# Performance work log

Hardware: AMD Instinct MI355X
Metric: run time of the kernel (lower is better)

## Reference

```python
import jax, jax.numpy as jnp
import numpy as np

N, E, D_IN, HID, D_OUT, HEADS = 4096, 262144, 256, 256, 128, 4


def gcn_conv(x, edge_index, edge_weight, W, b):
    # PyG GCNConv: linear -> gcn_norm (add self loops, sym norm) -> scatter-add -> +bias
    n = x.shape[0]
    row, col = edge_index[0], edge_index[1]
    loop = jnp.arange(n)
    row_f = jnp.concatenate([row, loop])
    col_f = jnp.concatenate([col, loop])
    ew_f = jnp.concatenate([edge_weight, jnp.ones((n,), edge_weight.dtype)])
    deg = jax.ops.segment_sum(ew_f, col_f, num_segments=n)
    dinv = jnp.where(deg > 0, jax.lax.rsqrt(deg), 0.0)
    norm = dinv[row_f] * ew_f * dinv[col_f]  # [E+N]
    h = x @ W                                # [N, out]
    out = jax.ops.segment_sum(norm[:, None] * h[row_f], col_f, num_segments=n)
    return out + b


def mha(x, in_proj_w, in_proj_b, out_proj_w, out_proj_b):
    # torch.nn.MultiheadAttention, unbatched input [L, Emb], q=k=v=x
    L, Emb = x.shape
    dh = Emb // HEADS
    qkv = x @ in_proj_w.T + in_proj_b
    q, k, v = jnp.split(qkv, 3, axis=-1)
    rs = lambda t: t.reshape(L, HEADS, dh).transpose(1, 0, 2)  # [H, L, dh]
    q, k, v = rs(q), rs(k), rs(v)
    scores = jnp.einsum('hld,hmd->hlm', q, k) / np.float32(np.sqrt(dh))
    attn = jax.nn.softmax(scores, axis=-1)
    o = jnp.einsum('hlm,hmd->hld', attn, v).transpose(1, 0, 2).reshape(L, Emb)
    return o @ out_proj_w.T + out_proj_b


def setup_inputs() -> dict:
    key = jax.random.key(0)
    ks = jax.random.split(key, 12)
    s = 0.02
    return {
        'node_features': jax.random.normal(ks[0], (N, D_IN), jnp.float32),
        'edge_index': jax.random.randint(ks[1], (2, E), 0, N),
        'edge_weight': jax.random.uniform(ks[2], (E,), jnp.float32),
        'W1': jax.random.normal(ks[3], (D_IN, HID), jnp.float32) * s,
        'b1': jnp.zeros((HID,), jnp.float32),
        'W2': jax.random.normal(ks[4], (HID, HID), jnp.float32) * s,
        'b2': jnp.zeros((HID,), jnp.float32),
        'W3': jax.random.normal(ks[5], (HID, D_OUT), jnp.float32) * s,
        'b3': jnp.zeros((D_OUT,), jnp.float32),
        'in_proj_w': jax.random.normal(ks[6], (3 * HID, HID), jnp.float32) * s,
        'in_proj_b': jnp.zeros((3 * HID,), jnp.float32),
        'out_proj_w': jax.random.normal(ks[7], (HID, HID), jnp.float32) * s,
        'out_proj_b': jnp.zeros((HID,), jnp.float32),
    }


def reference(node_features, edge_index, edge_weight, W1, b1, W2, b2, W3, b3,
              in_proj_w, in_proj_b, out_proj_w, out_proj_b):
    ew = edge_weight.astype(jnp.float32)
    x = gcn_conv(node_features, edge_index, ew, W1, b1)
    x = jax.nn.relu(mha(x, in_proj_w, in_proj_b, out_proj_w, out_proj_b))
    # dropout is identity at inference
    x = gcn_conv(x, edge_index, ew, W2, b2)
    x = jax.nn.relu(mha(x, in_proj_w, in_proj_b, out_proj_w, out_proj_b))
    x = gcn_conv(x, edge_index, ew, W3, b3)
    return jax.nn.sigmoid(x)
```

## Files before the change

### kernel.cpp

```cpp
#include <hip/hip_runtime.h>
#include <math.h>

#define N_NODES 4096
#define N_EDGES 262144

typedef __attribute__((ext_vector_type(4))) float f32x4;
typedef __attribute__((ext_vector_type(8))) short s16x8;
typedef __attribute__((ext_vector_type(4))) unsigned short u16x4;

__device__ inline unsigned short f2bf(float f) {
    unsigned u = __builtin_bit_cast(unsigned, f);
    u += 0x7FFF + ((u >> 16) & 1);
    return (unsigned short)(u >> 16);
}
__device__ inline unsigned short f2bf_t(float f) {
    return (unsigned short)(__builtin_bit_cast(unsigned, f) >> 16);
}
__device__ inline float bf2f(unsigned short u) {
    unsigned x = ((unsigned)u) << 16;
    return __builtin_bit_cast(float, x);
}

#define SWZ(row, colb) (((row) << 7) + ((colb) ^ (((row) & 7) << 4)))

__global__ void prep_all(const float* __restrict__ x0, const float* __restrict__ ipw,
                         const float* __restrict__ opw, const float* __restrict__ ipb,
                         const float* __restrict__ W1, const float* __restrict__ W2,
                         const float* __restrict__ W3,
                         unsigned short* __restrict__ x0b, unsigned short* __restrict__ ipwb,
                         unsigned short* __restrict__ opwb, float* __restrict__ ipbs,
                         unsigned short* __restrict__ W1t, unsigned short* __restrict__ W2t,
                         unsigned short* __restrict__ W3t) {
    const int NA = 262144;
    const int NB = 49152;
    const int NC = 16384;
    const int ND1 = 65536, ND2 = 65536, ND3 = 32768;
    const int NE = 768;
    const int total = NA + NB + NC + ND1 + ND2 + ND3 + NE;
    for (int idx = blockIdx.x * blockDim.x + threadIdx.x; idx < total;
         idx += gridDim.x * blockDim.x) {
        int t = idx;
        if (t < NA) {
            int i = t * 4;
            f32x4 v = *(const f32x4*)(x0 + i);
            u16x4 o;
#pragma unroll
            for (int j = 0; j < 4; j++) o[j] = f2bf(v[j]);
            *(u16x4*)(x0b + i) = o;
            continue;
        }
        t -= NA;
        if (t < NB) {
            int i = t * 4;
            int r = i >> 8;
            float sc = (r >= 256 && r < 512) ? 0.1803369f : 1.0f;
            f32x4 v = *(const f32x4*)(ipw + i);
            u16x4 o;
#pragma unroll
            for (int j = 0; j < 4; j++) o[j] = f2bf(v[j] * sc);
            *(u16x4*)(ipwb + i) = o;
            continue;
        }
        t -= NB;
        if (t < NC) {
            int i = t * 4;
            f32x4 v = *(const f32x4*)(opw + i);
            u16x4 o;
#pragma unroll
            for (int j = 0; j < 4; j++) o[j] = f2bf(v[j]);
            *(u16x4*)(opwb + i) = o;
            continue;
        }
        t -= NC;
        if (t < ND1) {
            int r = t & 255, c = t >> 8;
            W1t[c * 256 + r] = f2bf(W1[r * 256 + c]);
            continue;
        }
        t -= ND1;
        if (t < ND2) {
            int r = t & 255, c = t >> 8;
            W2t[c * 256 + r] = f2bf(W2[r * 256 + c]);
            continue;
        }
        t -= ND2;
        if (t < ND3) {
            int r = t & 255, c = t >> 8;
            W3t[c * 256 + r] = f2bf(W3[r * 128 + c]);
            continue;
        }
        t -= ND3;
        {
            float sc = (t >= 256 && t < 512) ? 0.1803369f : 1.0f;
            ipbs[t] = ipb[t] * sc;
        }
    }
}

__global__ void deg_accum(const int* __restrict__ col, const float* __restrict__ ew,
                          float* deg, int* cnt) {
    for (int e = blockIdx.x * blockDim.x + threadIdx.x; e < N_EDGES;
         e += gridDim.x * blockDim.x) {
        int c = col[e];
        atomicAdd(&deg[c], ew[e]);
        atomicAdd(&cnt[c], 1);
    }
}

__global__ __launch_bounds__(1024) void scan_offsets(const int* __restrict__ cnt,
                                                     float* __restrict__ deg,
                                                     int* off, int* fill) {
    __shared__ int s[1024];
    int tid = threadIdx.x;
#pragma unroll
    for (int q = 0; q < 4; q++) {
        int i = tid * 4 + q;
        deg[i] = rsqrtf(deg[i] + 1.0f);
    }
    int c0 = cnt[tid * 4 + 0], c1 = cnt[tid * 4 + 1];
    int c2 = cnt[tid * 4 + 2], c3 = cnt[tid * 4 + 3];
    int lsum = c0 + c1 + c2 + c3;
    s[tid] = lsum;
    __syncthreads();
    for (int d = 1; d < 1024; d <<= 1) {
        int v = (tid >= d) ? s[tid - d] : 0;
        __syncthreads();
        s[tid] += v;
        __syncthreads();
    }
    int incl = s[tid];
    int base = incl - lsum;
    int o0 = base, o1 = base + c0, o2 = base + c0 + c1, o3 = base + c0 + c1 + c2;
    off[tid * 4 + 0] = o0;  fill[tid * 4 + 0] = o0;
    off[tid * 4 + 1] = o1;  fill[tid * 4 + 1] = o1;
    off[tid * 4 + 2] = o2;  fill[tid * 4 + 2] = o2;
    off[tid * 4 + 3] = o3;  fill[tid * 4 + 3] = o3;
    if (tid == 1023) off[4096] = incl;
}

__global__ void scatter_edges(const int* __restrict__ row, const int* __restrict__ col,
                              const float* __restrict__ ew, const float* __restrict__ dinv,
                              int* fill, unsigned long long* __restrict__ ep) {
    for (int e = blockIdx.x * blockDim.x + threadIdx.x; e < N_EDGES;
         e += gridDim.x * blockDim.x) {
        int r = row[e], c = col[e];
        int p = atomicAdd(&fill[c], 1);
        float w = dinv[r] * ew[e] * dinv[c];
        unsigned long long v =
            ((unsigned long long)__builtin_bit_cast(unsigned, w) << 32) | (unsigned)r;
        ep[p] = v;
    }
}

template <bool BIAS, int ACT, bool QKV>
__global__ __launch_bounds__(64) void gemm_bf16(const unsigned short* __restrict__ A,
                                                const unsigned short* __restrict__ B,
                                                const float* __restrict__ bias,
                                                unsigned short* __restrict__ C,
                                                unsigned short* __restrict__ Vt, int P) {
    int lane = threadIdx.x & 63;
    int lx = lane & 15, g = lane >> 4;
    int brow = blockIdx.y * 32, bcol = blockIdx.x * 64;
    const unsigned short* Ap0 = A + (size_t)(brow + lx) * 256 + g * 8;
    const unsigned short* Ap1 = Ap0 + 16 * 256;
    const unsigned short* Bp = B + (size_t)(bcol + lx) * 256 + g * 8;
    f32x4 acc[2][4];
#pragma unroll
    for (int mi = 0; mi < 2; mi++)
#pragma unroll
        for (int nt = 0; nt < 4; nt++) acc[mi][nt] = f32x4{0.f, 0.f, 0.f, 0.f};
#pragma unroll
    for (int kc = 0; kc < 8; kc++) {
        s16x8 a0 = *(const s16x8*)(Ap0 + kc * 32);
        s16x8 a1 = *(const s16x8*)(Ap1 + kc * 32);
#pragma unroll
        for (int nt = 0; nt < 4; nt++) {
            s16x8 b = *(const s16x8*)(Bp + (size_t)nt * 16 * 256 + kc * 32);
            acc[0][nt] = __builtin_amdgcn_mfma_f32_16x16x32_bf16(a0, b, acc[0][nt], 0, 0, 0);
            acc[1][nt] = __builtin_amdgcn_mfma_f32_16x16x32_bf16(a1, b, acc[1][nt], 0, 0, 0);
        }
    }
    bool isV = QKV && (bcol >= 512);
    if (!isV) {
#pragma unroll
        for (int mi = 0; mi < 2; mi++)
#pragma unroll
            for (int nt = 0; nt < 4; nt++)
#pragma unroll
                for (int r = 0; r < 4; r++) {
                    int row = brow + mi * 16 + g * 4 + r, col = bcol + nt * 16 + lx;
                    float v = acc[mi][nt][r];
                    if (BIAS) v += bias[col];
                    if (ACT == 1) v = fmaxf(v, 0.f);
                    C[(size_t)row * P + col] = f2bf(v);
                }
    } else {
        int head = (bcol - 512) >> 6;
#pragma unroll
        for (int mi = 0; mi < 2; mi++)
#pragma unroll
            for (int nt = 0; nt < 4; nt++) {
                int col = bcol + nt * 16 + lx;
                u16x4 vv;
#pragma unroll
                for (int r = 0; r < 4; r++) {
                    float v = acc[mi][nt][r];
                    if (BIAS) v += bias[col];
                    vv[r] = f2bf(v);
                }
                *(u16x4*)(Vt + (size_t)(head * 64 + nt * 16 + lx) * 4096 +
                          brow + mi * 16 + g * 4) = vv;
            }
    }
}

template <int P, bool SIG>
__global__ __launch_bounds__(64) void gcn_agg(const unsigned short* __restrict__ H,
                                              const int* __restrict__ off,
                                              const unsigned long long* __restrict__ ep,
                                              const float* __restrict__ dinv,
                                              const float* __restrict__ bias,
                                              unsigned short* __restrict__ outb,
                                              float* __restrict__ outf) {
    constexpr int CPT = P / 64;
    __shared__ unsigned long long se[64];
    int i = blockIdx.x, tid = threadIdx.x;
    float di = dinv[i];
    float d2 = di * di;
    float acc[CPT];
    if (CPT == 4) {
        u16x4 h = *(const u16x4*)(H + (size_t)i * P + tid * 4);
#pragma unroll
        for (int j = 0; j < 4; j++) acc[j] = d2 * bf2f(h[j]);
    } else {
        unsigned h = *(const unsigned*)(H + (size_t)i * P + tid * 2);
        acc[0] = d2 * bf2f((unsigned short)(h & 0xFFFF));
        acc[1] = d2 * bf2f((unsigned short)(h >> 16));
    }
    int beg = off[i], end = off[i + 1];
    for (int base = beg; base < end; base += 64) {
        int n = min(64, end - base);
        __syncthreads();
        if (tid < n) se[tid] = ep[base + tid];
        __syncthreads();
#pragma unroll 4
        for (int j = 0; j < n; j++) {
            unsigned long long v = se[j];
            int r = (int)(unsigned)v;
            float w = __builtin_bit_cast(float, (unsigned)(v >> 32));
            size_t rb = (size_t)r * P;
            if (CPT == 4) {
                u16x4 h = *(const u16x4*)(H + rb + tid * 4);
#pragma unroll
                for (int q = 0; q < 4; q++) acc[q] += w * bf2f(h[q]);
            } else {
                unsigned h = *(const unsigned*)(H + rb + tid * 2);
                acc[0] += w * bf2f((unsigned short)(h & 0xFFFF));
                acc[1] += w * bf2f((unsigned short)(h >> 16));
            }
        }
    }
#pragma unroll
    for (int j = 0; j < CPT; j++) {
        int c = tid * CPT + j;
        float v = acc[j] + bias[c];
        if (SIG) {
            v = 1.f / (1.f + exp2f(-v * 1.442695f));
            outf[(size_t)i * P + c] = v;
        } else {
            outb[(size_t)i * P + c] = f2bf(v);
        }
    }
}

__global__ __launch_bounds__(256) void attn_mfma(const unsigned short* __restrict__ qkv,
                                                 const unsigned short* __restrict__ Vt,
                                                 unsigned short* __restrict__ Po,
                                                 float* __restrict__ Pl) {
    __shared__ unsigned short Ks[2][64 * 64];
    __shared__ unsigned short Vs[2][64 * 64];
    __shared__ unsigned short Ps[4][16 * 64];

    int tid = threadIdx.x;
    int wid = tid >> 6, lane = tid & 63, g = lane >> 4, lx = lane & 15;
    int head = blockIdx.y, chunk = blockIdx.z;
    int qw = blockIdx.x * 64 + wid * 16;

    s16x8 qa[2];
#pragma unroll
    for (int kc = 0; kc < 2; kc++)
        qa[kc] = *(const s16x8*)(qkv + (size_t)(qw + lx) * 768 + head * 64 + kc * 32 + g * 8);

    int kr0 = tid >> 3, dc0 = tid & 7;
    int kr1 = kr0 + 32;
    int kt_beg = chunk * 16, kt_end = kt_beg + 16;

    const unsigned short* kp0 =
        qkv + 256 + head * 64 + (size_t)(kt_beg * 64 + kr0) * 768 + dc0 * 8;
    const unsigned short* kp1 = kp0 + (size_t)32 * 768;
    const unsigned short* vp0 =
        Vt + (size_t)head * 64 * 4096 + (size_t)kr0 * 4096 + kt_beg * 64 + dc0 * 8;
    const unsigned short* vp1 = vp0 + (size_t)32 * 4096;

    s16x8 stK[2], stV[2];
    auto issue = [&]() {
        stK[0] = *(const s16x8*)kp0;
        stK[1] = *(const s16x8*)kp1;
        stV[0] = *(const s16x8*)vp0;
        stV[1] = *(const s16x8*)vp1;
        kp0 += 64 * 768; kp1 += 64 * 768;
        vp0 += 64; vp1 += 64;
    };
    auto commit = [&](int b) {
        *(s16x8*)((char*)Ks[b] + SWZ(kr0, dc0 * 16)) = stK[0];
        *(s16x8*)((char*)Ks[b] + SWZ(kr1, dc0 * 16)) = stK[1];
        *(s16x8*)((char*)Vs[b] + SWZ(kr0, dc0 * 16)) = stV[0];
        *(s16x8*)((char*)Vs[b] + SWZ(kr1, dc0 * 16)) = stV[1];
    };

    float lreg[4] = {0.f, 0.f, 0.f, 0.f};
    f32x4 o[4];
#pragma unroll
    for (int dt = 0; dt < 4; dt++) o[dt] = f32x4{0.f, 0.f, 0.f, 0.f};

    char* PsW = (char*)Ps[wid];

    issue();
    commit(0);
    __syncthreads();

    for (int kt = kt_beg; kt < kt_end; kt++) {
        int cur = (kt - kt_beg) & 1;
        if (kt + 1 < kt_end) issue();

        f32x4 s4[4];
        __builtin_amdgcn_s_setprio(1);
#pragma unroll
        for (int nt = 0; nt < 4; nt++) {
            f32x4 acc = f32x4{0.f, 0.f, 0.f, 0.f};
#pragma unroll
            for (int kc = 0; kc < 2; kc++) {
                s16x8 kb = *(const s16x8*)((char*)Ks[cur] + SWZ(nt * 16 + lx, kc * 64 + g * 16));
                acc = __builtin_amdgcn_mfma_f32_16x16x32_bf16(qa[kc], kb, acc, 0, 0, 0);
            }
            s4[nt] = acc;
        }
        __builtin_amdgcn_s_setprio(0);

#pragma unroll
        for (int nt = 0; nt < 4; nt++)
#pragma unroll
            for (int r = 0; r < 4; r++) {
                float p = exp2f(fminf(s4[nt][r], 60.f));
                lreg[r] += p;
                *(unsigned short*)(PsW + SWZ(4 * g + r, (nt * 16 + lx) * 2)) = f2bf_t(p);
            }

        __builtin_amdgcn_s_setprio(1);
#pragma unroll
        for (int kc = 0; kc < 2; kc++) {
            s16x8 pa = *(const s16x8*)(PsW + SWZ(lx, kc * 64 + g * 16));
#pragma unroll
            for (int dt = 0; dt < 4; dt++) {
                s16x8 vb = *(const s16x8*)((char*)Vs[cur] + SWZ(dt * 16 + lx, kc * 64 + g * 16));
                o[dt] = __builtin_amdgcn_mfma_f32_16x16x32_bf16(pa, vb, o[dt], 0, 0, 0);
            }
        }
        __builtin_amdgcn_s_setprio(0);

        if (kt + 1 < kt_end) commit(1 - cur);
        __syncthreads();
    }

#pragma unroll
    for (int r = 0; r < 4; r++) {
        float ls = lreg[r];
        ls += __shfl_xor(ls, 1, 16);
        ls += __shfl_xor(ls, 2, 16);
        ls += __shfl_xor(ls, 4, 16);
        ls += __shfl_xor(ls, 8, 16);
        int qrow = qw + 4 * g + r;
        size_t base = (size_t)(chunk * 4 + head) * 4096 + qrow;
        if (lx == 0) Pl[base] = ls;
#pragma unroll
        for (int dt = 0; dt < 4; dt++)
            Po[base * 64 + dt * 16 + lx] = f2bf(o[dt][r]);
    }
}

__global__ __launch_bounds__(256) void attn_combine(const unsigned short* __restrict__ Po,
                                                    const float* __restrict__ Pl,
                                                    unsigned short* __restrict__ att) {
    int tid = threadIdx.x;
    int q = blockIdx.x * 4 + (tid >> 6);
    int lane = tid & 63;
    int head = lane >> 4, quad = lane & 15;
    float L = 0.f;
    f32x4 ov = {0.f, 0.f, 0.f, 0.f};
#pragma unroll
    for (int c = 0; c < 4; c++) {
        size_t base = (size_t)(c * 4 + head) * 4096 + q;
        L += Pl[base];
        u16x4 p = *(const u16x4*)(Po + base * 64 + quad * 4);
#pragma unroll
        for (int k = 0; k < 4; k++) ov[k] += bf2f(p[k]);
    }
    float inv = 1.0f / L;
    u16x4 r;
#pragma unroll
    for (int k = 0; k < 4; k++) r[k] = f2bf(ov[k] * inv);
    *(u16x4*)(att + (size_t)q * 256 + head * 64 + quad * 4) = r;
}

extern "C" void kernel_launch(void* const* d_in, const int* in_sizes, int n_in,
                              void* d_out, int out_size, void* d_ws, size_t ws_size,
                              hipStream_t stream) {
    const float* x0  = (const float*)d_in[0];
    const int*   eix = (const int*)d_in[1];
    const float* ew  = (const float*)d_in[2];
    const float* W1  = (const float*)d_in[3];
    const float* b1  = (const float*)d_in[4];
    const float* W2  = (const float*)d_in[5];
    const float* b2  = (const float*)d_in[6];
    const float* W3  = (const float*)d_in[7];
    const float* b3  = (const float*)d_in[8];
    const float* ipw = (const float*)d_in[9];
    const float* ipb = (const float*)d_in[10];
    const float* opw = (const float*)d_in[11];
    const float* opb = (const float*)d_in[12];
    float* out = (float*)d_out;

    char* ws = (char*)d_ws;
    size_t o = 0;
    auto alloc = [&](size_t bytes) -> void* {
        void* p = ws + o;
        o = (o + bytes + 255) & ~size_t(255);
        return p;
    };
    float* dinv  = (float*)alloc(N_NODES * 4);
    int*   cnt   = (int*)alloc(N_NODES * 4);
    int*   off   = (int*)alloc((N_NODES + 1) * 4);
    int*   fill  = (int*)alloc(N_NODES * 4);
    unsigned long long* ep = (unsigned long long*)alloc((size_t)N_EDGES * 8);
    unsigned short* x0b  = (unsigned short*)alloc((size_t)N_NODES * 256 * 2);
    unsigned short* W1t  = (unsigned short*)alloc(256 * 256 * 2);
    unsigned short* W2t  = (unsigned short*)alloc(256 * 256 * 2);
    unsigned short* W3t  = (unsigned short*)alloc(128 * 256 * 2);
    unsigned short* ipwb = (unsigned short*)alloc(768 * 256 * 2);
    unsigned short* opwb = (unsigned short*)alloc(256 * 256 * 2);
    float* ipbs          = (float*)alloc(768 * 4);
    unsigned short* Hb   = (unsigned short*)alloc((size_t)N_NODES * 256 * 2);
    unsigned short* XAb  = (unsigned short*)alloc((size_t)N_NODES * 256 * 2);
    unsigned short* XBb  = (unsigned short*)alloc((size_t)N_NODES * 256 * 2);
    unsigned short* QKVb = (unsigned short*)alloc((size_t)N_NODES * 768 * 2);
    unsigned short* Vt   = (unsigned short*)alloc((size_t)4 * 64 * 4096 * 2);
    unsigned short* Po   = (unsigned short*)alloc((size_t)16 * 4096 * 64 * 2);
    float* Pl            = (float*)alloc((size_t)16 * 4096 * 4);

    const int* row = eix;
    const int* col = eix + N_EDGES;

    hipMemsetAsync(dinv, 0, N_NODES * 4, stream);
    hipMemsetAsync(cnt, 0, N_NODES * 4, stream);
    prep_all<<<512, 256, 0, stream>>>(x0, ipw, opw, ipb, W1, W2, W3,
                                      x0b, ipwb, opwb, ipbs, W1t, W2t, W3t);
    deg_accum<<<512, 256, 0, stream>>>(col, ew, dinv, cnt);
    scan_offsets<<<1, 1024, 0, stream>>>(cnt, dinv, off, fill);
    scatter_edges<<<512, 256, 0, stream>>>(row, col, ew, dinv, fill, ep);

    gemm_bf16<false, 0, false><<<dim3(4, 128), 64, 0, stream>>>(x0b, W1t, nullptr, Hb, nullptr, 256);
    gcn_agg<256, false><<<N_NODES, 64, 0, stream>>>(Hb, off, ep, dinv, b1, XAb, nullptr);
    gemm_bf16<true, 0, true><<<dim3(12, 128), 64, 0, stream>>>(XAb, ipwb, ipbs, QKVb, Vt, 768);
    attn_mfma<<<dim3(64, 4, 4), 256, 0, stream>>>(QKVb, Vt, Po, Pl);
    attn_combine<<<N_NODES / 4, 256, 0, stream>>>(Po, Pl, Hb);
    gemm_bf16<true, 1, false><<<dim3(4, 128), 64, 0, stream>>>(Hb, opwb, opb, XBb, nullptr, 256);
    gemm_bf16<false, 0, false><<<dim3(4, 128), 64, 0, stream>>>(XBb, W2t, nullptr, Hb, nullptr, 256);
    gcn_agg<256, false><<<N_NODES, 64, 0, stream>>>(Hb, off, ep, dinv, b2, XAb, nullptr);
    gemm_bf16<true, 0, true><<<dim3(12, 128), 64, 0, stream>>>(XAb, ipwb, ipbs, QKVb, Vt, 768);
    attn_mfma<<<dim3(64, 4, 4), 256, 0, stream>>>(QKVb, Vt, Po, Pl);
    attn_combine<<<N_NODES / 4, 256, 0, stream>>>(Po, Pl, Hb);
    gemm_bf16<true, 1, false><<<dim3(4, 128), 64, 0, stream>>>(Hb, opwb, opb, XBb, nullptr, 256);
    gemm_bf16<false, 0, false><<<dim3(2, 128), 64, 0, stream>>>(XBb, W3t, nullptr, Hb, nullptr, 128);
    gcn_agg<128, true><<<N_NODES, 64, 0, stream>>>(Hb, off, ep, dinv, b3, nullptr, out);
}
```

Before: 303.8 us.

## Fold degree accumulation into prep, enlarge GEMM tiles, split GCN edges across warps

Merges the degree/count atomic accumulation into the prep kernel to drop one launch. Enlarges the bf16 GEMM tile from 32 to 64 rows per single-wave block, halving the grid and reusing B fragments over four A fragments. Rewrites GCN aggregation to use four waves per node, each handling a strided subset of edges, followed by a shared-memory reduction. This trades fewer GEMM blocks and more register pressure for more memory-level parallelism in the gather.

```diff
diff --git a/kernel.cpp b/kernel.cpp
--- a/kernel.cpp
+++ b/kernel.cpp
@@ -27,16 +27,19 @@
                          const float* __restrict__ opw, const float* __restrict__ ipb,
                          const float* __restrict__ W1, const float* __restrict__ W2,
                          const float* __restrict__ W3,
+                         const int* __restrict__ col, const float* __restrict__ ew,
                          unsigned short* __restrict__ x0b, unsigned short* __restrict__ ipwb,
                          unsigned short* __restrict__ opwb, float* __restrict__ ipbs,
                          unsigned short* __restrict__ W1t, unsigned short* __restrict__ W2t,
-                         unsigned short* __restrict__ W3t) {
+                         unsigned short* __restrict__ W3t,
+                         float* __restrict__ deg, int* __restrict__ cnt) {
     const int NA = 262144;
     const int NB = 49152;
     const int NC = 16384;
     const int ND1 = 65536, ND2 = 65536, ND3 = 32768;
     const int NE = 768;
-    const int total = NA + NB + NC + ND1 + ND2 + ND3 + NE;
+    const int NG = N_EDGES;
+    const int total = NA + NB + NC + ND1 + ND2 + ND3 + NE + NG;
     for (int idx = blockIdx.x * blockDim.x + threadIdx.x; idx < total;
          idx += gridDim.x * blockDim.x) {
         int t = idx;
@@ -90,20 +93,17 @@
             continue;
         }
         t -= ND3;
-        {
+        if (t < NE) {
             float sc = (t >= 256 && t < 512) ? 0.1803369f : 1.0f;
             ipbs[t] = ipb[t] * sc;
-        }
-    }
-}
-
-__global__ void deg_accum(const int* __restrict__ col, const float* __restrict__ ew,
-                          float* deg, int* cnt) {
-    for (int e = blockIdx.x * blockDim.x + threadIdx.x; e < N_EDGES;
-         e += gridDim.x * blockDim.x) {
-        int c = col[e];
-        atomicAdd(&deg[c], ew[e]);
-        atomicAdd(&cnt[c], 1);
+            continue;
+        }
+        t -= NE;
+        {
+            int c = col[t];
+            atomicAdd(&deg[c], ew[t]);
+            atomicAdd(&cnt[c], 1);
+        }
     }
 }
 
@@ -160,30 +160,34 @@
                                                 unsigned short* __restrict__ Vt, int P) {
     int lane = threadIdx.x & 63;
     int lx = lane & 15, g = lane >> 4;
-    int brow = blockIdx.y * 32, bcol = blockIdx.x * 64;
-    const unsigned short* Ap0 = A + (size_t)(brow + lx) * 256 + g * 8;
-    const unsigned short* Ap1 = Ap0 + 16 * 256;
+    int brow = blockIdx.y * 64, bcol = blockIdx.x * 64;
+    const unsigned short* Ap = A + (size_t)(brow + lx) * 256 + g * 8;
     const unsigned short* Bp = B + (size_t)(bcol + lx) * 256 + g * 8;
-    f32x4 acc[2][4];
-#pragma unroll
-    for (int mi = 0; mi < 2; mi++)
+    f32x4 acc[4][4];
+#pragma unroll
+    for (int mi = 0; mi < 4; mi++)
 #pragma unroll
         for (int nt = 0; nt < 4; nt++) acc[mi][nt] = f32x4{0.f, 0.f, 0.f, 0.f};
 #pragma unroll
     for (int kc = 0; kc < 8; kc++) {
-        s16x8 a0 = *(const s16x8*)(Ap0 + kc * 32);
-        s16x8 a1 = *(const s16x8*)(Ap1 + kc * 32);
-#pragma unroll
-        for (int nt = 0; nt < 4; nt++) {
-            s16x8 b = *(const s16x8*)(Bp + (size_t)nt * 16 * 256 + kc * 32);
-            acc[0][nt] = __builtin_amdgcn_mfma_f32_16x16x32_bf16(a0, b, acc[0][nt], 0, 0, 0);
-            acc[1][nt] = __builtin_amdgcn_mfma_f32_16x16x32_bf16(a1, b, acc[1][nt], 0, 0, 0);
-        }
+        s16x8 a[4], b[4];
+#pragma unroll
+        for (int mi = 0; mi < 4; mi++)
+            a[mi] = *(const s16x8*)(Ap + (size_t)mi * 16 * 256 + kc * 32);
+#pragma unroll
+        for (int nt = 0; nt < 4; nt++)
+            b[nt] = *(const s16x8*)(Bp + (size_t)nt * 16 * 256 + kc * 32);
+#pragma unroll
+        for (int mi = 0; mi < 4; mi++)
+#pragma unroll
+            for (int nt = 0; nt < 4; nt++)
+                acc[mi][nt] = __builtin_amdgcn_mfma_f32_16x16x32_bf16(a[mi], b[nt],
+                                                                      acc[mi][nt], 0, 0, 0);
     }
     bool isV = QKV && (bcol >= 512);
     if (!isV) {
 #pragma unroll
-        for (int mi = 0; mi < 2; mi++)
+        for (int mi = 0; mi < 4; mi++)
 #pragma unroll
             for (int nt = 0; nt < 4; nt++)
 #pragma unroll
@@ -197,7 +201,7 @@
     } else {
         int head = (bcol - 512) >> 6;
 #pragma unroll
-        for (int mi = 0; mi < 2; mi++)
+        for (int mi = 0; mi < 4; mi++)
 #pragma unroll
             for (int nt = 0; nt < 4; nt++) {
                 int col = bcol + nt * 16 + lx;
@@ -215,60 +219,72 @@
 }
 
 template <int P, bool SIG>
-__global__ __launch_bounds__(64) void gcn_agg(const unsigned short* __restrict__ H,
-                                              const int* __restrict__ off,
-                                              const unsigned long long* __restrict__ ep,
-                                              const float* __restrict__ dinv,
-                                              const float* __restrict__ bias,
-                                              unsigned short* __restrict__ outb,
-                                              float* __restrict__ outf) {
+__global__ __launch_bounds__(256) void gcn_agg(const unsigned short* __restrict__ H,
+                                               const int* __restrict__ off,
+                                               const unsigned long long* __restrict__ ep,
+                                               const float* __restrict__ dinv,
+                                               const float* __restrict__ bias,
+                                               unsigned short* __restrict__ outb,
+                                               float* __restrict__ outf) {
     constexpr int CPT = P / 64;
-    __shared__ unsigned long long se[64];
+    __shared__ unsigned long long se[128];
+    __shared__ float red[3][P];
     int i = blockIdx.x, tid = threadIdx.x;
-    float di = dinv[i];
-    float d2 = di * di;
+    int wid = tid >> 6, lane = tid & 63;
     float acc[CPT];
-    if (CPT == 4) {
-        u16x4 h = *(const u16x4*)(H + (size_t)i * P + tid * 4);
-#pragma unroll
-        for (int j = 0; j < 4; j++) acc[j] = d2 * bf2f(h[j]);
-    } else {
-        unsigned h = *(const unsigned*)(H + (size_t)i * P + tid * 2);
-        acc[0] = d2 * bf2f((unsigned short)(h & 0xFFFF));
-        acc[1] = d2 * bf2f((unsigned short)(h >> 16));
+#pragma unroll
+    for (int j = 0; j < CPT; j++) acc[j] = 0.f;
+    if (wid == 0) {
+        float di = dinv[i];
+        float d2 = di * di;
+        if (CPT == 4) {
+            u16x4 h = *(const u16x4*)(H + (size_t)i * P + lane * 4);
+#pragma unroll
+            for (int j = 0; j < 4; j++) acc[j] = d2 * bf2f(h[j]);
+        } else {
+            unsigned h = *(const unsigned*)(H + (size_t)i * P + lane * 2);
+            acc[0] = d2 * bf2f((unsigned short)(h & 0xFFFF));
+            acc[1] = d2 * bf2f((unsigned short)(h >> 16));
+        }
     }
     int beg = off[i], end = off[i + 1];
-    for (int base = beg; base < end; base += 64) {
-        int n = min(64, end - base);
+    for (int base = beg; base < end; base += 128) {
+        int n = min(128, end - base);
         __syncthreads();
         if (tid < n) se[tid] = ep[base + tid];
         __syncthreads();
-#pragma unroll 4
-        for (int j = 0; j < n; j++) {
+        for (int j = wid; j < n; j += 4) {
             unsigned long long v = se[j];
             int r = (int)(unsigned)v;
             float w = __builtin_bit_cast(float, (unsigned)(v >> 32));
             size_t rb = (size_t)r * P;
             if (CPT == 4) {
-                u16x4 h = *(const u16x4*)(H + rb + tid * 4);
+                u16x4 h = *(const u16x4*)(H + rb + lane * 4);
 #pragma unroll
                 for (int q = 0; q < 4; q++) acc[q] += w * bf2f(h[q]);
             } else {
-                unsigned h = *(const unsigned*)(H + rb + tid * 2);
+                unsigned h = *(const unsigned*)(H + rb + lane * 2);
                 acc[0] += w * bf2f((unsigned short)(h & 0xFFFF));
                 acc[1] += w * bf2f((unsigned short)(h >> 16));
             }
         }
     }
-#pragma unroll
-    for (int j = 0; j < CPT; j++) {
-        int c = tid * CPT + j;
-        float v = acc[j] + bias[c];
-        if (SIG) {
-            v = 1.f / (1.f + exp2f(-v * 1.442695f));
-            outf[(size_t)i * P + c] = v;
-        } else {
-            outb[(size_t)i * P + c] = f2bf(v);
+    if (wid > 0) {
+#pragma unroll
+        for (int j = 0; j < CPT; j++) red[wid - 1][lane * CPT + j] = acc[j];
+    }
+    __syncthreads();
+    if (wid == 0) {
+#pragma unroll
+        for (int j = 0; j < CPT; j++) {
+            int c = lane * CPT + j;
+            float v = acc[j] + red[0][c] + red[1][c] + red[2][c] + bias[c];
+            if (SIG) {
+                v = 1.f / (1.f + exp2f(-v * 1.442695f));
+                outf[(size_t)i * P + c] = v;
+            } else {
+                outb[(size_t)i * P + c] = f2bf(v);
+            }
         }
     }
 }
@@ -462,24 +478,23 @@
 
     hipMemsetAsync(dinv, 0, N_NODES * 4, stream);
     hipMemsetAsync(cnt, 0, N_NODES * 4, stream);
-    prep_all<<<512, 256, 0, stream>>>(x0, ipw, opw, ipb, W1, W2, W3,
-                                      x0b, ipwb, opwb, ipbs, W1t, W2t, W3t);
-    deg_accum<<<512, 256, 0, stream>>>(col, ew, dinv, cnt);
+    prep_all<<<512, 256, 0, stream>>>(x0, ipw, opw, ipb, W1, W2, W3, col, ew,
+                                      x0b, ipwb, opwb, ipbs, W1t, W2t, W3t, dinv, cnt);
     scan_offsets<<<1, 1024, 0, stream>>>(cnt, dinv, off, fill);
     scatter_edges<<<512, 256, 0, stream>>>(row, col, ew, dinv, fill, ep);
 
-    gemm_bf16<false, 0, false><<<dim3(4, 128), 64, 0, stream>>>(x0b, W1t, nullptr, Hb, nullptr, 256);
-    gcn_agg<256, false><<<N_NODES, 64, 0, stream>>>(Hb, off, ep, dinv, b1, XAb, nullptr);
-    gemm_bf16<true, 0, true><<<dim3(12, 128), 64, 0, stream>>>(XAb, ipwb, ipbs, QKVb, Vt, 768);
+    gemm_bf16<false, 0, false><<<dim3(4, 64), 64, 0, stream>>>(x0b, W1t, nullptr, Hb, nullptr, 256);
+    gcn_agg<256, false><<<N_NODES, 256, 0, stream>>>(Hb, off, ep, dinv, b1, XAb, nullptr);
+    gemm_bf16<true, 0, true><<<dim3(12, 64), 64, 0, stream>>>(XAb, ipwb, ipbs, QKVb, Vt, 768);
     attn_mfma<<<dim3(64, 4, 4), 256, 0, stream>>>(QKVb, Vt, Po, Pl);
     attn_combine<<<N_NODES / 4, 256, 0, stream>>>(Po, Pl, Hb);
-    gemm_bf16<true, 1, false><<<dim3(4, 128), 64, 0, stream>>>(Hb, opwb, opb, XBb, nullptr, 256);
-    gemm_bf16<false, 0, false><<<dim3(4, 128), 64, 0, stream>>>(XBb, W2t, nullptr, Hb, nullptr, 256);
-    gcn_agg<256, false><<<N_NODES, 64, 0, stream>>>(Hb, off, ep, dinv, b2, XAb, nullptr);
-    gemm_bf16<true, 0, true><<<dim3(12, 128), 64, 0, stream>>>(XAb, ipwb, ipbs, QKVb, Vt, 768);
+    gemm_bf16<true, 1, false><<<dim3(4, 64), 64, 0, stream>>>(Hb, opwb, opb, XBb, nullptr, 256);
+    gemm_bf16<false, 0, false><<<dim3(4, 64), 64, 0, stream>>>(XBb, W2t, nullptr, Hb, nullptr, 256);
+    gcn_agg<256, false><<<N_NODES, 256, 0, stream>>>(Hb, off, ep, dinv, b2, XAb, nullptr);
+    gemm_bf16<true, 0, true><<<dim3(12, 64), 64, 0, stream>>>(XAb, ipwb, ipbs, QKVb, Vt, 768);
     attn_mfma<<<dim3(64, 4, 4), 256, 0, stream>>>(QKVb, Vt, Po, Pl);
     attn_combine<<<N_NODES / 4, 256, 0, stream>>>(Po, Pl, Hb);
-    gemm_bf16<true, 1, false><<<dim3(4, 128), 64, 0, stream>>>(Hb, opwb, opb, XBb, nullptr, 256);
-    gemm_bf16<false, 0, false><<<dim3(2, 128), 64, 0, stream>>>(XBb, W3t, nullptr, Hb, nullptr, 128);
-    gcn_agg<128, true><<<N_NODES, 64, 0, stream>>>(Hb, off, ep, dinv, b3, nullptr, out);
-}
+    gemm_bf16<true, 1, false><<<dim3(4, 64), 64, 0, stream>>>(Hb, opwb, opb, XBb, nullptr, 256);
+    gemm_bf16<false, 0, false><<<dim3(2, 64), 64, 0, stream>>>(XBb, W3t, nullptr, Hb, nullptr, 128);
+    gcn_agg<128, true><<<N_NODES, 256, 0, stream>>>(Hb, off, ep, dinv, b3, nullptr, out);
+}
```

Measured after the change: 316.5 us. 4.2% more time.

## Fuse attention combine into out-projection GEMM, remap attention grid for XCDs

Applied to the files above, without the earlier changes.

The split-K attention combine (summing the partial outputs and normalising by the softmax sums) moves into the A-operand load of a new out-projection GEMM kernel with fused bias and ReLU. This drops one kernel launch and the write and re-read of the intermediate attention buffer per MHA layer. Separately, the attention grid is flattened and remapped so blocks sharing a head and chunk land on the same XCD, which should improve L2 reuse of K and V. The two memsets are folded into prep_all, and gcn_agg stages 128 edges per batch instead of 64. In exchange, the fused GEMM re-reads the partial outputs once per column block (four times) and writes its output with scalar stores.

```diff
diff --git a/kernel.cpp b/kernel.cpp
--- a/kernel.cpp
+++ b/kernel.cpp
@@ -30,13 +30,15 @@
                          unsigned short* __restrict__ x0b, unsigned short* __restrict__ ipwb,
                          unsigned short* __restrict__ opwb, float* __restrict__ ipbs,
                          unsigned short* __restrict__ W1t, unsigned short* __restrict__ W2t,
-                         unsigned short* __restrict__ W3t) {
+                         unsigned short* __restrict__ W3t,
+                         float* __restrict__ deg, int* __restrict__ cnt) {
     const int NA = 262144;
     const int NB = 49152;
     const int NC = 16384;
     const int ND1 = 65536, ND2 = 65536, ND3 = 32768;
     const int NE = 768;
-    const int total = NA + NB + NC + ND1 + ND2 + ND3 + NE;
+    const int NF = 4096;
+    const int total = NA + NB + NC + ND1 + ND2 + ND3 + NE + NF;
     for (int idx = blockIdx.x * blockDim.x + threadIdx.x; idx < total;
          idx += gridDim.x * blockDim.x) {
         int t = idx;
@@ -90,10 +92,14 @@
             continue;
         }
         t -= ND3;
-        {
+        if (t < NE) {
             float sc = (t >= 256 && t < 512) ? 0.1803369f : 1.0f;
             ipbs[t] = ipb[t] * sc;
-        }
+            continue;
+        }
+        t -= NE;
+        deg[t] = 0.f;
+        cnt[t] = 0;
     }
 }
 
@@ -214,6 +220,72 @@
     }
 }
 
+__global__ __launch_bounds__(64) void gemm_op(const unsigned short* __restrict__ Po,
+                                              const float* __restrict__ Pl,
+                                              const unsigned short* __restrict__ B,
+                                              const float* __restrict__ bias,
+                                              unsigned short* __restrict__ C) {
+    int lane = threadIdx.x & 63;
+    int lx = lane & 15, g = lane >> 4;
+    int brow = blockIdx.y * 32, bcol = blockIdx.x * 64;
+    int rows[2] = {brow + lx, brow + 16 + lx};
+    float Linv[2][4];
+#pragma unroll
+    for (int mi = 0; mi < 2; mi++)
+#pragma unroll
+        for (int h = 0; h < 4; h++) {
+            float L = 0.f;
+#pragma unroll
+            for (int c = 0; c < 4; c++)
+                L += Pl[(size_t)(c * 4 + h) * 4096 + rows[mi]];
+            Linv[mi][h] = 1.0f / L;
+        }
+    const unsigned short* Bp = B + (size_t)(bcol + lx) * 256 + g * 8;
+    f32x4 acc[2][4];
+#pragma unroll
+    for (int mi = 0; mi < 2; mi++)
+#pragma unroll
+        for (int nt = 0; nt < 4; nt++) acc[mi][nt] = f32x4{0.f, 0.f, 0.f, 0.f};
+#pragma unroll
+    for (int kc = 0; kc < 8; kc++) {
+        int k0 = kc * 32 + g * 8;
+        int h = k0 >> 6, d0 = k0 & 63;
+        s16x8 a[2];
+#pragma unroll
+        for (int mi = 0; mi < 2; mi++) {
+            float sum[8] = {0.f, 0.f, 0.f, 0.f, 0.f, 0.f, 0.f, 0.f};
+#pragma unroll
+            for (int c = 0; c < 4; c++) {
+                s16x8 p = *(const s16x8*)(Po +
+                    ((size_t)(c * 4 + h) * 4096 + rows[mi]) * 64 + d0);
+#pragma unroll
+                for (int j = 0; j < 8; j++) sum[j] += bf2f((unsigned short)p[j]);
+            }
+            s16x8 av;
+            float li = Linv[mi][h];
+#pragma unroll
+            for (int j = 0; j < 8; j++) av[j] = (short)f2bf(sum[j] * li);
+            a[mi] = av;
+        }
+#pragma unroll
+        for (int nt = 0; nt < 4; nt++) {
+            s16x8 b = *(const s16x8*)(Bp + (size_t)nt * 16 * 256 + kc * 32);
+            acc[0][nt] = __builtin_amdgcn_mfma_f32_16x16x32_bf16(a[0], b, acc[0][nt], 0, 0, 0);
+            acc[1][nt] = __builtin_amdgcn_mfma_f32_16x16x32_bf16(a[1], b, acc[1][nt], 0, 0, 0);
+        }
+    }
+#pragma unroll
+    for (int mi = 0; mi < 2; mi++)
+#pragma unroll
+        for (int nt = 0; nt < 4; nt++)
+#pragma unroll
+            for (int r = 0; r < 4; r++) {
+                int row = brow + mi * 16 + g * 4 + r, col = bcol + nt * 16 + lx;
+                float v = fmaxf(acc[mi][nt][r] + bias[col], 0.f);
+                C[(size_t)row * 256 + col] = f2bf(v);
+            }
+}
+
 template <int P, bool SIG>
 __global__ __launch_bounds__(64) void gcn_agg(const unsigned short* __restrict__ H,
                                               const int* __restrict__ off,
@@ -223,7 +295,7 @@
                                               unsigned short* __restrict__ outb,
                                               float* __restrict__ outf) {
     constexpr int CPT = P / 64;
-    __shared__ unsigned long long se[64];
+    __shared__ unsigned long long se[128];
     int i = blockIdx.x, tid = threadIdx.x;
     float di = dinv[i];
     float d2 = di * di;
@@ -238,10 +310,11 @@
         acc[1] = d2 * bf2f((unsigned short)(h >> 16));
     }
     int beg = off[i], end = off[i + 1];
-    for (int base = beg; base < end; base += 64) {
-        int n = min(64, end - base);
+    for (int base = beg; base < end; base += 128) {
+        int n = min(128, end - base);
         __syncthreads();
         if (tid < n) se[tid] = ep[base + tid];
+        if (tid + 64 < n) se[tid + 64] = ep[base + tid + 64];
         __syncthreads();
 #pragma unroll 4
         for (int j = 0; j < n; j++) {
@@ -283,8 +356,12 @@
 
     int tid = threadIdx.x;
     int wid = tid >> 6, lane = tid & 63, g = lane >> 4, lx = lane & 15;
-    int head = blockIdx.y, chunk = blockIdx.z;
-    int qw = blockIdx.x * 64 + wid * 16;
+    int bid = blockIdx.x;
+    int xcd = bid & 7, loc = bid >> 3;
+    int pair = xcd * 2 + (loc >> 6);
+    int qt = loc & 63;
+    int head = pair >> 2, chunk = pair & 3;
+    int qw = qt * 64 + wid * 16;
 
     s16x8 qa[2];
 #pragma unroll
@@ -308,7 +385,7 @@
         stK[1] = *(const s16x8*)kp1;
         stV[0] = *(const s16x8*)vp0;
         stV[1] = *(const s16x8*)vp1;
-        kp0 += 64 * 768; kp1 += 64 * 768;
+        kp0 += (size_t)64 * 768; kp1 += (size_t)64 * 768;
         vp0 += 64; vp1 += 64;
     };
     auto commit = [&](int b) {
@@ -386,30 +463,6 @@
         for (int dt = 0; dt < 4; dt++)
             Po[base * 64 + dt * 16 + lx] = f2bf(o[dt][r]);
     }
-}
-
-__global__ __launch_bounds__(256) void attn_combine(const unsigned short* __restrict__ Po,
-                                                    const float* __restrict__ Pl,
-                                                    unsigned short* __restrict__ att) {
-    int tid = threadIdx.x;
-    int q = blockIdx.x * 4 + (tid >> 6);
-    int lane = tid & 63;
-    int head = lane >> 4, quad = lane & 15;
-    float L = 0.f;
-    f32x4 ov = {0.f, 0.f, 0.f, 0.f};
-#pragma unroll
-    for (int c = 0; c < 4; c++) {
-        size_t base = (size_t)(c * 4 + head) * 4096 + q;
-        L += Pl[base];
-        u16x4 p = *(const u16x4*)(Po + base * 64 + quad * 4);
-#pragma unroll
-        for (int k = 0; k < 4; k++) ov[k] += bf2f(p[k]);
-    }
-    float inv = 1.0f / L;
-    u16x4 r;
-#pragma unroll
-    for (int k = 0; k < 4; k++) r[k] = f2bf(ov[k] * inv);
-    *(u16x4*)(att + (size_t)q * 256 + head * 64 + quad * 4) = r;
 }
 
 extern "C" void kernel_launch(void* const* d_in, const int* in_sizes, int n_in,
@@ -460,10 +513,8 @@
     const int* row = eix;
     const int* col = eix + N_EDGES;
 
-    hipMemsetAsync(dinv, 0, N_NODES * 4, stream);
-    hipMemsetAsync(cnt, 0, N_NODES * 4, stream);
     prep_all<<<512, 256, 0, stream>>>(x0, ipw, opw, ipb, W1, W2, W3,
-                                      x0b, ipwb, opwb, ipbs, W1t, W2t, W3t);
+                                      x0b, ipwb, opwb, ipbs, W1t, W2t, W3t, dinv, cnt);
     deg_accum<<<512, 256, 0, stream>>>(col, ew, dinv, cnt);
     scan_offsets<<<1, 1024, 0, stream>>>(cnt, dinv, off, fill);
     scatter_edges<<<512, 256, 0, stream>>>(row, col, ew, dinv, fill, ep);
@@ -471,15 +522,13 @@
     gemm_bf16<false, 0, false><<<dim3(4, 128), 64, 0, stream>>>(x0b, W1t, nullptr, Hb, nullptr, 256);
     gcn_agg<256, false><<<N_NODES, 64, 0, stream>>>(Hb, off, ep, dinv, b1, XAb, nullptr);
     gemm_bf16<true, 0, true><<<dim3(12, 128), 64, 0, stream>>>(XAb, ipwb, ipbs, QKVb, Vt, 768);
-    attn_mfma<<<dim3(64, 4, 4), 256, 0, stream>>>(QKVb, Vt, Po, Pl);
-    attn_combine<<<N_NODES / 4, 256, 0, stream>>>(Po, Pl, Hb);
-    gemm_bf16<true, 1, false><<<dim3(4, 128), 64, 0, stream>>>(Hb, opwb, opb, XBb, nullptr, 256);
+    attn_mfma<<<1024, 256, 0, stream>>>(QKVb, Vt, Po, Pl);
+    gemm_op<<<dim3(4, 128), 64, 0, stream>>>(Po, Pl, opwb, opb, XBb);
     gemm_bf16<false, 0, false><<<dim3(4, 128), 64, 0, stream>>>(XBb, W2t, nullptr, Hb, nullptr, 256);
     gcn_agg<256, false><<<N_NODES, 64, 0, stream>>>(Hb, off, ep, dinv, b2, XAb, nullptr);
     gemm_bf16<true, 0, true><<<dim3(12, 128), 64, 0, stream>>>(XAb, ipwb, ipbs, QKVb, Vt, 768);
-    attn_mfma<<<dim3(64, 4, 4), 256, 0, stream>>>(QKVb, Vt, Po, Pl);
-    attn_combine<<<N_NODES / 4, 256, 0, stream>>>(Po, Pl, Hb);
-    gemm_bf16<true, 1, false><<<dim3(4, 128), 64, 0, stream>>>(Hb, opwb, opb, XBb, nullptr, 256);
+    attn_mfma<<<1024, 256, 0, stream>>>(QKVb, Vt, Po, Pl);
+    gemm_op<<<dim3(4, 128), 64, 0, stream>>>(Po, Pl, opwb, opb, XBb);
     gemm_bf16<false, 0, false><<<dim3(2, 128), 64, 0, stream>>>(XBb, W3t, nullptr, Hb, nullptr, 128);
     gcn_agg<128, true><<<N_NODES, 64, 0, stream>>>(Hb, off, ep, dinv, b3, nullptr, out);
 }
```

Measured after the change: 301.3 us. Within noise of the previous version (-0.8%).
